# Kernel tuning notes

Hardware: AMD Instinct MI355X
Metric: run time of the kernel (lower is better)

Reference implementation:

```python
import jax, jax.numpy as jnp
import numpy as np

WINDOW = 16
VD = 6
HID = 16


def setup_inputs() -> dict:
    key = jax.random.key(0)
    ks = jax.random.split(key, 10)
    B, S = 256, 4096
    sc = 0.1
    return {
        "x": jax.random.normal(ks[0], (B, S, 2), jnp.float32),
        "h_0": jnp.zeros((B, HID), jnp.float32),
        "fir_I_w": jax.random.normal(ks[1], (VD, WINDOW), jnp.float32) * sc,
        "fir_Q_w": jax.random.normal(ks[2], (VD, WINDOW), jnp.float32) * sc,
        "W_fi_w": jax.random.normal(ks[3], (HID, 2 * VD), jnp.float32) * sc,
        "W_fi_b": jnp.zeros((HID,), jnp.float32),
        "W_fh_w": jax.random.normal(ks[4], (HID, HID), jnp.float32) * sc,
        "W_gi_w": jax.random.normal(ks[5], (HID, 2 * VD), jnp.float32) * sc,
        "W_gi_b": jnp.zeros((HID,), jnp.float32),
        "W_gh_w": jax.random.normal(ks[6], (HID, HID), jnp.float32) * sc,
        "W_out_I_w": jax.random.normal(ks[7], (1, HID), jnp.float32) * sc,
        "W_out_I_b": jnp.zeros((1,), jnp.float32),
        "W_out_Q_w": jax.random.normal(ks[8], (1, HID), jnp.float32) * sc,
        "W_out_Q_b": jnp.zeros((1,), jnp.float32),
    }


def _tile_theta(t, hidden):
    # pr_block replication logic for vd_units < hidden <= 3*vd_units cases
    if VD >= hidden:
        return t[..., :hidden]
    elif hidden <= 2 * VD:
        return jnp.concatenate([t, t[..., : hidden - VD]], axis=-1)
    else:
        return jnp.concatenate([t, t, t[..., : hidden - 2 * VD]], axis=-1)


def reference(x, h_0, fir_I_w, fir_Q_w, W_fi_w, W_fi_b, W_fh_w,
              W_gi_w, W_gi_b, W_gh_w, W_out_I_w, W_out_I_b,
              W_out_Q_w, W_out_Q_b):
    B, S, _ = x.shape
    # Causal sliding windows: window at t covers x[t-15 .. t] with zero pad.
    xp = jnp.concatenate([jnp.zeros((B, WINDOW - 1, 2), x.dtype), x], axis=1)
    idx = jnp.arange(S)[:, None] + jnp.arange(WINDOW)[None, :]  # (S, W)
    win = xp[:, idx, :]  # (B, S, W, 2)
    wI, wQ = win[..., 0], win[..., 1]  # (B, S, W)
    # Complex FIR filter
    I_fir = jnp.einsum('bsw,vw->bsv', wI, fir_I_w) - jnp.einsum('bsw,vw->bsv', wQ, fir_Q_w)
    Q_fir = jnp.einsum('bsw,vw->bsv', wI, fir_Q_w) + jnp.einsum('bsw,vw->bsv', wQ, fir_I_w)
    mag = jnp.sqrt(I_fir * I_fir + Q_fir * Q_fir) + 1e-8
    mag2 = mag * mag
    sin_t = Q_fir / mag
    cos_t = I_fir / mag
    # L = stack([mag, mag2], dim=2).view(B, S, 2*VD)
    L = jnp.stack([mag, mag2], axis=2).reshape(B, S, 2 * VD)
    # Precompute input contributions to gates; scan the recurrence.
    fi = jnp.einsum('bsl,hl->bsh', L, W_fi_w) + W_fi_b  # (B,S,H)
    gi = jnp.einsum('bsl,hl->bsh', L, W_gi_w) + W_gi_b

    def step(h, inp):
        fi_t, gi_t = inp
        f = jax.nn.sigmoid(fi_t + h @ W_fh_w.T)
        g = jnp.tanh(gi_t + h @ W_gh_w.T)
        h = f * h + (1.0 - f) * g
        return h, h

    _, h_seq = jax.lax.scan(step, h_0, (fi.transpose(1, 0, 2), gi.transpose(1, 0, 2)))
    h_seq = h_seq.transpose(1, 0, 2)  # (B, S, H)
    hidden = h_seq.shape[-1]
    cos_r = _tile_theta(cos_t, hidden)
    sin_r = _tile_theta(sin_t, hidden)
    I_rot = h_seq * cos_r
    Q_rot = h_seq * sin_r
    oI = I_rot @ W_out_I_w.T + W_out_I_b  # (B,S,1)
    oQ = Q_rot @ W_out_Q_w.T + W_out_Q_b
    out_I = oI - oQ
    out_Q = oQ + oI
    return jnp.concatenate([out_I, out_Q], axis=-1)
```

## Files before the change

kernel.cpp:

```cpp
#include <hip/hip_runtime.h>
#include <stdint.h>

#define DEV __device__ __forceinline__

constexpr int Bb   = 256;
constexpr int Ss   = 4096;
constexpr int HIDN = 16;
constexpr int VDN  = 6;
constexpr int WINN = 16;

constexpr int BPG   = 32;
constexpr int NG    = Bb / BPG;
constexpr int CHUNK = 16;
constexpr int WARM  = 16;
constexpr int NCH   = Ss / CHUNK;
constexpr int NPH   = (CHUNK + WARM) / 4;
constexpr int EPH   = WARM / 4;

constexpr size_t WSL_BYTES = (size_t)NG * Ss * 64 * 16;
constexpr size_t WSC_BYTES = (size_t)NG * Ss * BPG * 24;

typedef __fp16 h2v  __attribute__((ext_vector_type(2)));
typedef __fp16 f16x8 __attribute__((ext_vector_type(8)));
typedef float  f32x16 __attribute__((ext_vector_type(16)));

DEV uint32_t pk16(float a, float b) {
    h2v t = __builtin_amdgcn_cvt_pkrtz(a, b);
    uint32_t u; __builtin_memcpy(&u, &t, 4); return u;
}
DEV void up16(uint32_t u, float& a, float& b) {
    h2v t; __builtin_memcpy(&t, &u, 4);
    a = (float)t[0]; b = (float)t[1];
}
DEV f32x16 MF(const uint32_t* a, const uint32_t* b, f32x16 c) {
    f16x8 av, bv;
    __builtin_memcpy(&av, a, 16);
    __builtin_memcpy(&bv, b, 16);
    return __builtin_amdgcn_mfma_f32_32x32x16_f16(av, bv, c, 0, 0, 0);
}

template<int C> DEV int   dpp_i(int v)  { return __builtin_amdgcn_update_dpp(0, v, C, 0xF, 0xF, false); }
template<int C> DEV float dpp_f(float v){ return __int_as_float(dpp_i<C>(__float_as_int(v))); }
#define DPP_ALL(X) X(1,0x121) X(2,0x122) X(3,0x123) X(4,0x124) X(5,0x125) X(6,0x126) X(7,0x127) \
  X(8,0x128) X(9,0x129) X(10,0x12A) X(11,0x12B) X(12,0x12C) X(13,0x12D) X(14,0x12E) X(15,0x12F)

__global__ __launch_bounds__(256, 4) void boja_front(
    const float* __restrict__ x,
    const float* __restrict__ fIw, const float* __restrict__ fQw,
    uint4* __restrict__ wsl, uint2* __restrict__ wsc)
{
    __shared__ __align__(16) uint32_t lds[8 * 64 * 4];
    const int tid = threadIdx.x;
    const int tq  = tid & 7;
    const int b_  = tid >> 3;
    const int G   = blockIdx.y;
    const int t0  = blockIdx.x * 8;
    const int t   = t0 + tq;
    const int b   = G * BPG + b_;
    const int id  = b * Ss + t;
    const float2* x2 = (const float2*)x;

    float wI[WINN], wQ[WINN];
    if (t >= WINN - 1) {
#pragma unroll
        for (int w = 0; w < WINN; ++w) { float2 v = x2[id - 15 + w]; wI[w] = v.x; wQ[w] = v.y; }
    } else {
#pragma unroll
        for (int w = 0; w < WINN; ++w) {
            int ts = t - 15 + w;
            float2 v = (ts >= 0) ? x2[id - 15 + w] : make_float2(0.f, 0.f);
            wI[w] = v.x; wQ[w] = v.y;
        }
    }
    float aI[VDN], aQ[VDN];
#pragma unroll
    for (int v = 0; v < VDN; ++v) { aI[v] = 0.f; aQ[v] = 0.f; }
#pragma unroll
    for (int w = 0; w < WINN; ++w) {
#pragma unroll
        for (int v = 0; v < VDN; ++v) {
            aI[v] = fmaf( wI[w], fIw[v*16+w], aI[v]);
            aI[v] = fmaf(-wQ[w], fQw[v*16+w], aI[v]);
            aQ[v] = fmaf( wI[w], fQw[v*16+w], aQ[v]);
            aQ[v] = fmaf( wQ[w], fIw[v*16+w], aQ[v]);
        }
    }
    float L[12];
    uint32_t sc[6];
#pragma unroll
    for (int v = 0; v < VDN; ++v) {
        float m2 = fmaf(aI[v], aI[v], aQ[v]*aQ[v]);
        float mg = __builtin_amdgcn_sqrtf(m2) + 1e-8f;
        float iv = __builtin_amdgcn_rcpf(mg);
        L[v] = mg; L[6+v] = mg*mg;
        sc[v] = pk16(aI[v]*iv, aQ[v]*iv);
    }
    {
        const size_t cb = ((size_t)(G * Ss + t) * BPG + b_) * 3;
        wsc[cb+0] = make_uint2(sc[0], sc[1]);
        wsc[cb+1] = make_uint2(sc[2], sc[3]);
        wsc[cb+2] = make_uint2(sc[4], sc[5]);
    }
    const int lo = (tq*64 + b_) * 4, hi = (tq*64 + b_ + 32) * 4;
    lds[lo+0] = pk16(L[0], L[1]);  lds[lo+1] = pk16(L[2],  L[3]);
    lds[lo+2] = pk16(L[8], L[9]);  lds[lo+3] = pk16(L[10], L[11]);
    lds[hi+0] = pk16(L[4], L[5]);  lds[hi+1] = pk16(L[6],  L[7]);
    lds[hi+2] = 0x00003C00u;
    lds[hi+3] = 0u;
    __syncthreads();
#pragma unroll
    for (int r = 0; r < 2; ++r) {
        int idx = r*256 + tid;
        int tq2 = idx >> 6, lane = idx & 63;
        uint4 v = *(const uint4*)&lds[(tq2*64 + lane)*4];
        wsl[(size_t)(G*Ss + t0 + tq2) * 64 + lane] = v;
    }
}

__global__ __launch_bounds__(64, 2) void boja_rnn(
    const uint4* __restrict__ wsl, const uint2* __restrict__ wsc,
    const float* __restrict__ h0,
    const float* __restrict__ Wfh, const float* __restrict__ Wgh,
    const float* __restrict__ Wfi, const float* __restrict__ bfi,
    const float* __restrict__ Wgi, const float* __restrict__ bgi,
    const float* __restrict__ WoI, const float* __restrict__ boI,
    const float* __restrict__ WoQ, const float* __restrict__ boQ,
    float* __restrict__ out)
{
    const int l  = threadIdx.x;
    const int b_ = l & 31;
    const int h_ = l >> 5;
    const int G  = blockIdx.x & (NG - 1);
    const int ci = blockIdx.x >> 3;

    const int t_out0  = ci * CHUNK;
    const int t_start = t_out0 - WARM;
    const bool useh0  = (t_start <= 0);

    const float CF = -1.4426950408889634f;
    const float CG =  2.8853900817779268f;
    const int   m  = b_;
    const float sA = (m < 16) ? CF : CG;

    uint32_t a1[4], a2[4];
#pragma unroll
    for (int d = 0; d < 4; ++d) {
        float wv[2], uv[2];
#pragma unroll
        for (int q = 0; q < 2; ++q) {
            const int e = d*2 + q;
            const int k = (e & 3) + 8*(e >> 2) + 4*h_;
            wv[q] = ((m < 16) ? Wfh[m*16 + k] : Wgh[(m-16)*16 + k]) * sA;
            float u;
            if (k < 12)       u = ((m < 16) ? Wfi[m*12 + k] : Wgi[(m-16)*12 + k]) * sA;
            else if (k == 12) u = ((m < 16) ? bfi[m] : bgi[m-16]) * sA;
            else              u = 0.0f;
            uv[q] = u;
        }
        a1[d] = pk16(wv[0], wv[1]);
        a2[d] = pk16(uv[0], uv[1]);
    }

    float woi[8], woq[8];
#pragma unroll
    for (int r = 0; r < 8; ++r) {
        const int j = (r & 3) + 8*(r >> 2) + 4*h_;
        woi[r] = WoI[j]; woq[r] = WoQ[j];
    }
    const float bo_i = boI[0], bo_q = boQ[0];

    float h0r[8];
    if (useh0) {
        const float* hp = h0 + (size_t)(G*BPG + b_) * HIDN;
        float4 p = *(const float4*)(hp + 4*h_);
        float4 q = *(const float4*)(hp + 8 + 4*h_);
        h0r[0]=p.x; h0r[1]=p.y; h0r[2]=p.z; h0r[3]=p.w;
        h0r[4]=q.x; h0r[5]=q.y; h0r[6]=q.z; h0r[7]=q.w;
    }
    float hreg[8];
#pragma unroll
    for (int r = 0; r < 8; ++r) hreg[r] = 0.0f;
    uint32_t b1[4];
    b1[0]=0u; b1[1]=0u; b1[2]=0u; b1[3]=0u;

    f32x16 zero16;
#pragma unroll
    for (int i = 0; i < 16; ++i) zero16[i] = 0.0f;

    const uint4* lp = wsl + (size_t)G * Ss * 64 + l;
    const uint2* cp = wsc + ((size_t)G * Ss * BPG + b_) * 3;
    float2* outp = (float2*)out + (size_t)(G*BPG + b_) * Ss;

    uint4 LB[3][4];
    uint2 CB[2][4][3];

    auto loadL = [&](uint4 (&B)[4], int tb) {
#pragma unroll
        for (int s = 0; s < 4; ++s) {
            int tq2 = tb + s; tq2 = (tq2 < 0) ? 0 : tq2;
            B[s] = lp[(size_t)tq2 * 64];
        }
    };
    auto loadC = [&](uint2 (&C)[4][3], int tb) {
#pragma unroll
        for (int s = 0; s < 4; ++s)
#pragma unroll
            for (int k = 0; k < 3; ++k)
                C[s][k] = cp[(size_t)(tb + s) * (BPG*3) + k];
    };

    loadL(LB[0], t_start);
    loadL(LB[1], t_start + 4);

#define PHASE(P) { \
    const int tb = t_start + 4*(P); \
    if ((P) + 2 < NPH) loadL(LB[((P)+2)%3], t_start + 4*((P)+2)); \
    if ((P) + 1 >= EPH && (P) + 1 < NPH) loadC(CB[((P)+1)&1], t_start + 4*((P)+1)); \
    f32x16 accL = MF(a2, (const uint32_t*)&LB[(P)%3][0], zero16); \
    float ob[8]; \
    _Pragma("unroll") \
    for (int s = 0; s < 4; ++s) { \
        if (useh0 && tb + s == 0) { \
            _Pragma("unroll") for (int r = 0; r < 8; ++r) hreg[r] = h0r[r]; \
            b1[0]=pk16(hreg[0],hreg[1]); b1[1]=pk16(hreg[2],hreg[3]); \
            b1[2]=pk16(hreg[4],hreg[5]); b1[3]=pk16(hreg[6],hreg[7]); \
        } \
        f32x16 acc = MF(a1, b1, accL); \
        if (s < 3) accL = MF(a2, (const uint32_t*)&LB[(P)%3][s+1], zero16); \
        _Pragma("unroll") \
        for (int r = 0; r < 8; ++r) { \
            float f = __builtin_amdgcn_rcpf(1.0f + __builtin_amdgcn_exp2f(acc[r])); \
            float g = fmaf(-2.0f, __builtin_amdgcn_rcpf(1.0f + __builtin_amdgcn_exp2f(acc[r+8])), 1.0f); \
            hreg[r] = fmaf(f, hreg[r] - g, g); \
        } \
        b1[0]=pk16(hreg[0],hreg[1]); b1[1]=pk16(hreg[2],hreg[3]); \
        b1[2]=pk16(hreg[4],hreg[5]); b1[3]=pk16(hreg[6],hreg[7]); \
        if ((P) >= EPH) { \
            float cs6[6], sn6[6]; \
            up16(CB[(P)&1][s][0].x, cs6[0], sn6[0]); up16(CB[(P)&1][s][0].y, cs6[1], sn6[1]); \
            up16(CB[(P)&1][s][1].x, cs6[2], sn6[2]); up16(CB[(P)&1][s][1].y, cs6[3], sn6[3]); \
            up16(CB[(P)&1][s][2].x, cs6[4], sn6[4]); up16(CB[(P)&1][s][2].y, cs6[5], sn6[5]); \
            float oI = bo_i, oQ = bo_q; \
            const bool hb = (h_ != 0); \
            { \
                float c0,sn0; \
                c0 = hb?cs6[4]:cs6[0]; sn0 = hb?sn6[4]:sn6[0]; oI = fmaf(hreg[0]*c0, woi[0], oI); oQ = fmaf(hreg[0]*sn0, woq[0], oQ); \
                c0 = hb?cs6[5]:cs6[1]; sn0 = hb?sn6[5]:sn6[1]; oI = fmaf(hreg[1]*c0, woi[1], oI); oQ = fmaf(hreg[1]*sn0, woq[1], oQ); \
                c0 = hb?cs6[0]:cs6[2]; sn0 = hb?sn6[0]:sn6[2]; oI = fmaf(hreg[2]*c0, woi[2], oI); oQ = fmaf(hreg[2]*sn0, woq[2], oQ); \
                c0 = hb?cs6[1]:cs6[3]; sn0 = hb?sn6[1]:sn6[3]; oI = fmaf(hreg[3]*c0, woi[3], oI); oQ = fmaf(hreg[3]*sn0, woq[3], oQ); \
                c0 = hb?cs6[0]:cs6[2]; sn0 = hb?sn6[0]:sn6[2]; oI = fmaf(hreg[4]*c0, woi[4], oI); oQ = fmaf(hreg[4]*sn0, woq[4], oQ); \
                c0 = hb?cs6[1]:cs6[3]; sn0 = hb?sn6[1]:sn6[3]; oI = fmaf(hreg[5]*c0, woi[5], oI); oQ = fmaf(hreg[5]*sn0, woq[5], oQ); \
                c0 = hb?cs6[2]:cs6[4]; sn0 = hb?sn6[2]:sn6[4]; oI = fmaf(hreg[6]*c0, woi[6], oI); oQ = fmaf(hreg[6]*sn0, woq[6], oQ); \
                c0 = hb?cs6[3]:cs6[5]; sn0 = hb?sn6[3]:sn6[5]; oI = fmaf(hreg[7]*c0, woi[7], oI); oQ = fmaf(hreg[7]*sn0, woq[7], oQ); \
            } \
            oI += __shfl_xor(oI, 32, 64); \
            oQ += __shfl_xor(oQ, 32, 64); \
            ob[s*2] = oI - oQ; ob[s*2+1] = oI + oQ; \
        } \
    } \
    if ((P) >= EPH && l < 32) { \
        float4* po = (float4*)(outp + tb); \
        po[0] = make_float4(ob[0], ob[1], ob[2], ob[3]); \
        po[1] = make_float4(ob[4], ob[5], ob[6], ob[7]); \
    } \
}

    PHASE(0)  PHASE(1)  PHASE(2)  PHASE(3)
    PHASE(4)  PHASE(5)  PHASE(6)  PHASE(7)
#undef PHASE
}

__global__ __launch_bounds__(64, 2) void bojanet_v2(
    const float* __restrict__ x,   const float* __restrict__ h0,
    const float* __restrict__ fIw, const float* __restrict__ fQw,
    const float* __restrict__ Wfi, const float* __restrict__ bfi,
    const float* __restrict__ Wfh, const float* __restrict__ Wgi,
    const float* __restrict__ bgi, const float* __restrict__ Wgh,
    const float* __restrict__ WoI, const float* __restrict__ boI,
    const float* __restrict__ WoQ, const float* __restrict__ boQ,
    float* __restrict__ out)
{
    constexpr int FCH = 128, FWR = 64, FSB = 16;
    __shared__ __align__(16) float s_fi[FSB * 80];
    __shared__ __align__(16) float s_gi[FSB * 80];
    __shared__ __align__(16) float s_h [FSB * 68];
    __shared__ float s_sc[4 * 12 * 17];

    const int lane = threadIdx.x;
    const int j  = lane & 15;
    const int bl = lane >> 4;
    const int ci = blockIdx.x;
    const int b0 = blockIdx.y * 4;
    const int t_out0  = ci * FCH;
    const int t_start = ci ? (t_out0 - FWR) : 0;
    const int t_end   = t_out0 + FCH;

    int c[16]; c[0] = j;
#define CSET(K,CTL) c[K] = dpp_i<CTL>(j);
    DPP_ALL(CSET)
#undef CSET
    float wf[16], wg[16];
#pragma unroll
    for (int k = 0; k < 16; ++k) { wf[k] = Wfh[j*16 + c[k]]; wg[k] = Wgh[j*16 + c[k]]; }

    float h = (ci == 0) ? h0[(b0 + bl) * HIDN + j] : 0.0f;
    const float2* x2   = (const float2*)x + (size_t)(b0 + bl) * Ss;
    float2*       out2 = (float2*)out     + (size_t)(b0 + bl) * Ss;

    for (int tb = t_start; tb < t_end; tb += FSB) {
        const bool emit = (tb >= t_out0);
        {
            const int tg = tb + j;
            float wI[WINN], wQ[WINN];
            if (tb >= WINN - 1) {
#pragma unroll
                for (int w = 0; w < WINN; ++w) { float2 v = x2[tg - 15 + w]; wI[w] = v.x; wQ[w] = v.y; }
            } else {
#pragma unroll
                for (int w = 0; w < WINN; ++w) {
                    int ts = tg - 15 + w;
                    float2 v = (ts >= 0) ? x2[ts] : make_float2(0.f, 0.f);
                    wI[w] = v.x; wQ[w] = v.y;
                }
            }
            float aI[VDN], aQ[VDN];
#pragma unroll
            for (int v = 0; v < VDN; ++v) { aI[v] = 0.f; aQ[v] = 0.f; }
#pragma unroll
            for (int w = 0; w < WINN; ++w) {
#pragma unroll
                for (int v = 0; v < VDN; ++v) {
                    aI[v] = fmaf( wI[w], fIw[v*16+w], aI[v]);
                    aI[v] = fmaf(-wQ[w], fQw[v*16+w], aI[v]);
                    aQ[v] = fmaf( wI[w], fQw[v*16+w], aQ[v]);
                    aQ[v] = fmaf( wQ[w], fIw[v*16+w], aQ[v]);
                }
            }
            float L[12];
#pragma unroll
            for (int v = 0; v < VDN; ++v) {
                float m2 = fmaf(aI[v], aI[v], aQ[v]*aQ[v]);
                float mg = __builtin_amdgcn_sqrtf(m2) + 1e-8f;
                L[v] = mg; L[6+v] = mg*mg;
                if (emit) {
                    float iv = __builtin_amdgcn_rcpf(mg);
                    s_sc[(bl*12 + v  )*17 + j] = aI[v] * iv;
                    s_sc[(bl*12 + 6+v)*17 + j] = aQ[v] * iv;
                }
            }
            float fi[16], gi[16];
#pragma unroll
            for (int k = 0; k < 16; ++k) { fi[k] = bfi[k]; gi[k] = bgi[k]; }
#pragma unroll
            for (int ll = 0; ll < 12; ++ll) {
#pragma unroll
                for (int k = 0; k < 16; ++k) {
                    fi[k] = fmaf(L[ll], Wfi[k*12+ll], fi[k]);
                    gi[k] = fmaf(L[ll], Wgi[k*12+ll], gi[k]);
                }
            }
            float* pf = &s_fi[j*80 + bl*20];
            float* pg = &s_gi[j*80 + bl*20];
#pragma unroll
            for (int q = 0; q < 4; ++q) {
                *(float4*)(pf + 4*q) = make_float4(fi[4*q], fi[4*q+1], fi[4*q+2], fi[4*q+3]);
                *(float4*)(pg + 4*q) = make_float4(gi[4*q], gi[4*q+1], gi[4*q+2], gi[4*q+3]);
            }
        }
        __asm__ volatile("s_waitcnt lgkmcnt(0)" ::: "memory");
        {
            const int rb = bl*20 + j;
            float pf0 = s_fi[rb], pf1 = s_fi[80 + rb];
            float pg0 = s_gi[rb], pg1 = s_gi[80 + rb];
#pragma unroll
            for (int tt = 0; tt < FSB; ++tt) {
                const int nx = (tt + 2 < FSB) ? tt + 2 : FSB - 1;
                float pfn = s_fi[nx*80 + rb];
                float pgn = s_gi[nx*80 + rb];
                float hr[16]; hr[0] = h;
#define HSET(K,CTL) hr[K] = dpp_f<CTL>(h);
                DPP_ALL(HSET)
#undef HSET
                float af0 = pf0, af1 = 0.f, ag0 = pg0, ag1 = 0.f;
#pragma unroll
                for (int k = 0; k < 8; ++k) {
                    af0 = fmaf(wf[k],   hr[k],   af0);
                    ag0 = fmaf(wg[k],   hr[k],   ag0);
                    af1 = fmaf(wf[k+8], hr[k+8], af1);
                    ag1 = fmaf(wg[k+8], hr[k+8], ag1);
                }
                float zf = af0 + af1, zg = ag0 + ag1;
                float f = __builtin_amdgcn_rcpf(1.0f + __builtin_amdgcn_exp2f(zf * -1.4426950408889634f));
                float g = fmaf(-2.0f, __builtin_amdgcn_rcpf(1.0f + __builtin_amdgcn_exp2f(zg * 2.8853900817779268f)), 1.0f);
                h = fmaf(f, h - g, g);
                s_h[tt*68 + bl*16 + j] = h;
                pf0 = pf1; pf1 = pfn; pg0 = pg1; pg1 = pgn;
            }
        }
        __asm__ volatile("s_waitcnt lgkmcnt(0)" ::: "memory");
        if (emit) {
            const int tg = tb + j;
            float hv[16];
#pragma unroll
            for (int q = 0; q < 4; ++q) {
                float4 t4 = *(const float4*)&s_h[j*68 + bl*16 + 4*q];
                hv[4*q] = t4.x; hv[4*q+1] = t4.y; hv[4*q+2] = t4.z; hv[4*q+3] = t4.w;
            }
            float cs[12];
#pragma unroll
            for (int k = 0; k < 12; ++k) cs[k] = s_sc[(bl*12 + k)*17 + j];
            float oI = boI[0], oQ = boQ[0];
#pragma unroll
            for (int k = 0; k < 16; ++k) {
                int v = (k < 6) ? k : ((k < 12) ? k - 6 : k - 12);
                oI = fmaf(hv[k]*cs[v],   WoI[k], oI);
                oQ = fmaf(hv[k]*cs[6+v], WoQ[k], oQ);
            }
            out2[tg] = make_float2(oI - oQ, oI + oQ);
        }
        __asm__ volatile("s_waitcnt lgkmcnt(0)" ::: "memory");
    }
}

extern "C" void kernel_launch(void* const* d_in, const int* in_sizes, int n_in,
                              void* d_out, int out_size, void* d_ws, size_t ws_size,
                              hipStream_t stream) {
    const float* x   = (const float*)d_in[0];
    const float* h0  = (const float*)d_in[1];
    const float* fIw = (const float*)d_in[2];
    const float* fQw = (const float*)d_in[3];
    const float* Wfi = (const float*)d_in[4];
    const float* bfi = (const float*)d_in[5];
    const float* Wfh = (const float*)d_in[6];
    const float* Wgi = (const float*)d_in[7];
    const float* bgi = (const float*)d_in[8];
    const float* Wgh = (const float*)d_in[9];
    const float* WoI = (const float*)d_in[10];
    const float* boI = (const float*)d_in[11];
    const float* WoQ = (const float*)d_in[12];
    const float* boQ = (const float*)d_in[13];
    float* out = (float*)d_out;

    if (ws_size >= WSL_BYTES + WSC_BYTES) {
        uint4* wsl = (uint4*)d_ws;
        uint2* wsc = (uint2*)((char*)d_ws + WSL_BYTES);
        boja_front<<<dim3(Ss/8, NG), 256, 0, stream>>>(x, fIw, fQw, wsl, wsc);
        boja_rnn<<<dim3(NG * NCH), 64, 0, stream>>>(
            wsl, wsc, h0, Wfh, Wgh, Wfi, bfi, Wgi, bgi, WoI, boI, WoQ, boQ, out);
    } else {
        bojanet_v2<<<dim3(32, Bb / 4), 64, 0, stream>>>(
            x, h0, fIw, fQw, Wfi, bfi, Wfh, Wgi, bgi, Wgh, WoI, boI, WoQ, boQ, out);
    }
}
```

Measured before the change: 48.83 us.

## Switch RNN recurrence to 16x16x32 MFMA with 16-batch groups and compact workspace

Replaces the 32x32x16 MFMA recurrence (32 batches per wave, f and g gates stacked) with 16x16x32 MFMAs over 16 batches per wave, issuing separate f and g MFMAs. The front kernel now writes a tighter fp16 workspace (48 uint2 per timestep instead of 64 uint4) and stages the cos/sin data through LDS so global writes are coalesced. Doubling the group count doubles the number of RNN blocks, giving more parallel waves for the latency-bound sequential chain. The cost is four MFMAs per step instead of two, plus an extra shuffle stage in the output reduction.

```diff
diff --git a/kernel.cpp b/kernel.cpp
--- a/kernel.cpp
+++ b/kernel.cpp
@@ -9,7 +9,7 @@
 constexpr int VDN  = 6;
 constexpr int WINN = 16;
 
-constexpr int BPG   = 32;
+constexpr int BPG   = 16;
 constexpr int NG    = Bb / BPG;
 constexpr int CHUNK = 16;
 constexpr int WARM  = 16;
@@ -17,12 +17,12 @@
 constexpr int NPH   = (CHUNK + WARM) / 4;
 constexpr int EPH   = WARM / 4;
 
-constexpr size_t WSL_BYTES = (size_t)NG * Ss * 64 * 16;
+constexpr size_t WSL_BYTES = (size_t)NG * Ss * 48 * 8;
 constexpr size_t WSC_BYTES = (size_t)NG * Ss * BPG * 24;
 
-typedef __fp16 h2v  __attribute__((ext_vector_type(2)));
+typedef __fp16 h2v   __attribute__((ext_vector_type(2)));
 typedef __fp16 f16x8 __attribute__((ext_vector_type(8)));
-typedef float  f32x16 __attribute__((ext_vector_type(16)));
+typedef float  f32x4 __attribute__((ext_vector_type(4)));
 
 DEV uint32_t pk16(float a, float b) {
     h2v t = __builtin_amdgcn_cvt_pkrtz(a, b);
@@ -32,11 +32,11 @@
     h2v t; __builtin_memcpy(&t, &u, 4);
     a = (float)t[0]; b = (float)t[1];
 }
-DEV f32x16 MF(const uint32_t* a, const uint32_t* b, f32x16 c) {
+DEV f32x4 MF16(const uint32_t* a, const uint32_t* b, f32x4 c) {
     f16x8 av, bv;
     __builtin_memcpy(&av, a, 16);
     __builtin_memcpy(&bv, b, 16);
-    return __builtin_amdgcn_mfma_f32_32x32x16_f16(av, bv, c, 0, 0, 0);
+    return __builtin_amdgcn_mfma_f32_16x16x32_f16(av, bv, c, 0, 0, 0);
 }
 
 template<int C> DEV int   dpp_i(int v)  { return __builtin_amdgcn_update_dpp(0, v, C, 0xF, 0xF, false); }
@@ -44,18 +44,20 @@
 #define DPP_ALL(X) X(1,0x121) X(2,0x122) X(3,0x123) X(4,0x124) X(5,0x125) X(6,0x126) X(7,0x127) \
   X(8,0x128) X(9,0x129) X(10,0x12A) X(11,0x12B) X(12,0x12C) X(13,0x12D) X(14,0x12E) X(15,0x12F)
 
-__global__ __launch_bounds__(256, 4) void boja_front(
+__global__ __launch_bounds__(256, 4) void boja_front16(
     const float* __restrict__ x,
     const float* __restrict__ fIw, const float* __restrict__ fQw,
-    uint4* __restrict__ wsl, uint2* __restrict__ wsc)
+    uint2* __restrict__ wsl, uint2* __restrict__ wsc)
 {
-    __shared__ __align__(16) uint32_t lds[8 * 64 * 4];
+    __shared__ __align__(8) uint2 lsl[16 * 48];
+    __shared__ __align__(8) uint2 lsc[16 * 48];
+
     const int tid = threadIdx.x;
-    const int tq  = tid & 7;
-    const int b_  = tid >> 3;
+    const int tl  = tid & 15;
+    const int b_  = tid >> 4;
     const int G   = blockIdx.y;
-    const int t0  = blockIdx.x * 8;
-    const int t   = t0 + tq;
+    const int t0  = blockIdx.x * 16;
+    const int t   = t0 + tl;
     const int b   = G * BPG + b_;
     const int id  = b * Ss + t;
     const float2* x2 = (const float2*)x;
@@ -85,40 +87,34 @@
             aQ[v] = fmaf( wQ[w], fIw[v*16+w], aQ[v]);
         }
     }
-    float L[12];
-    uint32_t sc[6];
+    float mg[VDN], mq[VDN];
+    uint32_t sc[VDN];
 #pragma unroll
     for (int v = 0; v < VDN; ++v) {
         float m2 = fmaf(aI[v], aI[v], aQ[v]*aQ[v]);
-        float mg = __builtin_amdgcn_sqrtf(m2) + 1e-8f;
-        float iv = __builtin_amdgcn_rcpf(mg);
-        L[v] = mg; L[6+v] = mg*mg;
+        mg[v] = __builtin_amdgcn_sqrtf(m2) + 1e-8f;
+        mq[v] = mg[v] * mg[v];
+        float iv = __builtin_amdgcn_rcpf(mg[v]);
         sc[v] = pk16(aI[v]*iv, aQ[v]*iv);
     }
-    {
-        const size_t cb = ((size_t)(G * Ss + t) * BPG + b_) * 3;
-        wsc[cb+0] = make_uint2(sc[0], sc[1]);
-        wsc[cb+1] = make_uint2(sc[2], sc[3]);
-        wsc[cb+2] = make_uint2(sc[4], sc[5]);
-    }
-    const int lo = (tq*64 + b_) * 4, hi = (tq*64 + b_ + 32) * 4;
-    lds[lo+0] = pk16(L[0], L[1]);  lds[lo+1] = pk16(L[2],  L[3]);
-    lds[lo+2] = pk16(L[8], L[9]);  lds[lo+3] = pk16(L[10], L[11]);
-    lds[hi+0] = pk16(L[4], L[5]);  lds[hi+1] = pk16(L[6],  L[7]);
-    lds[hi+2] = 0x00003C00u;
-    lds[hi+3] = 0u;
+    lsl[tl*48 +  0 + b_] = make_uint2(pk16(mg[0], mg[1]), pk16(mg[2], mg[3]));
+    lsl[tl*48 + 16 + b_] = make_uint2(pk16(mg[4], mg[5]), pk16(mq[0], mq[1]));
+    lsl[tl*48 + 32 + b_] = make_uint2(pk16(mq[2], mq[3]), pk16(mq[4], mq[5]));
+    lsc[tl*48 + b_*3 + 0] = make_uint2(sc[0], sc[1]);
+    lsc[tl*48 + b_*3 + 1] = make_uint2(sc[2], sc[3]);
+    lsc[tl*48 + b_*3 + 2] = make_uint2(sc[4], sc[5]);
     __syncthreads();
 #pragma unroll
-    for (int r = 0; r < 2; ++r) {
+    for (int r = 0; r < 3; ++r) {
         int idx = r*256 + tid;
-        int tq2 = idx >> 6, lane = idx & 63;
-        uint4 v = *(const uint4*)&lds[(tq2*64 + lane)*4];
-        wsl[(size_t)(G*Ss + t0 + tq2) * 64 + lane] = v;
-    }
-}
-
-__global__ __launch_bounds__(64, 2) void boja_rnn(
-    const uint4* __restrict__ wsl, const uint2* __restrict__ wsc,
+        int tq2 = idx / 48, e = idx - tq2*48;
+        wsl[(size_t)(G*Ss + t0 + tq2) * 48 + e] = lsl[idx];
+        wsc[(size_t)(G*Ss + t0 + tq2) * 48 + e] = lsc[idx];
+    }
+}
+
+__global__ __launch_bounds__(64, 4) void boja_rnn16(
+    const uint2* __restrict__ wsl, const uint2* __restrict__ wsc,
     const float* __restrict__ h0,
     const float* __restrict__ Wfh, const float* __restrict__ Wgh,
     const float* __restrict__ Wfi, const float* __restrict__ bfi,
@@ -128,10 +124,10 @@
     float* __restrict__ out)
 {
     const int l  = threadIdx.x;
-    const int b_ = l & 31;
-    const int h_ = l >> 5;
+    const int b_ = l & 15;
+    const int q  = l >> 4;
     const int G  = blockIdx.x & (NG - 1);
-    const int ci = blockIdx.x >> 3;
+    const int ci = blockIdx.x >> 4;
 
     const int t_out0  = ci * CHUNK;
     const int t_start = t_out0 - WARM;
@@ -139,74 +135,60 @@
 
     const float CF = -1.4426950408889634f;
     const float CG =  2.8853900817779268f;
-    const int   m  = b_;
-    const float sA = (m < 16) ? CF : CG;
-
-    uint32_t a1[4], a2[4];
-#pragma unroll
-    for (int d = 0; d < 4; ++d) {
-        float wv[2], uv[2];
-#pragma unroll
-        for (int q = 0; q < 2; ++q) {
-            const int e = d*2 + q;
-            const int k = (e & 3) + 8*(e >> 2) + 4*h_;
-            wv[q] = ((m < 16) ? Wfh[m*16 + k] : Wgh[(m-16)*16 + k]) * sA;
-            float u;
-            if (k < 12)       u = ((m < 16) ? Wfi[m*12 + k] : Wgi[(m-16)*12 + k]) * sA;
-            else if (k == 12) u = ((m < 16) ? bfi[m] : bgi[m-16]) * sA;
-            else              u = 0.0f;
-            uv[q] = u;
-        }
-        a1[d] = pk16(wv[0], wv[1]);
-        a2[d] = pk16(uv[0], uv[1]);
-    }
-
-    float woi[8], woq[8];
-#pragma unroll
-    for (int r = 0; r < 8; ++r) {
-        const int j = (r & 3) + 8*(r >> 2) + 4*h_;
-        woi[r] = WoI[j]; woq[r] = WoQ[j];
-    }
+
+    uint32_t a1f[4] = {0,0,0,0}, a1g[4] = {0,0,0,0};
+    uint32_t a2f[4] = {0,0,0,0}, a2g[4] = {0,0,0,0};
+    const int m_ = b_;
+#pragma unroll
+    for (int d = 0; d < 2; ++d) {
+        const int k0 = 4*q + 2*d, k1 = k0 + 1;
+        a1f[d] = pk16(Wfh[m_*16 + k0]*CF, Wfh[m_*16 + k1]*CF);
+        a1g[d] = pk16(Wgh[m_*16 + k0]*CG, Wgh[m_*16 + k1]*CG);
+        auto uf = [&](int k)->float { return (k < 12) ? Wfi[m_*12 + k] : ((k == 12) ? bfi[m_] : 0.f); };
+        auto ug = [&](int k)->float { return (k < 12) ? Wgi[m_*12 + k] : ((k == 12) ? bgi[m_] : 0.f); };
+        a2f[d] = pk16(uf(k0)*CF, uf(k1)*CF);
+        a2g[d] = pk16(ug(k0)*CG, ug(k1)*CG);
+    }
+
+    float woi[4], woq[4];
+#pragma unroll
+    for (int r = 0; r < 4; ++r) { woi[r] = WoI[4*q + r]; woq[r] = WoQ[4*q + r]; }
     const float bo_i = boI[0], bo_q = boQ[0];
 
-    float h0r[8];
+    float h0r[4];
     if (useh0) {
-        const float* hp = h0 + (size_t)(G*BPG + b_) * HIDN;
-        float4 p = *(const float4*)(hp + 4*h_);
-        float4 q = *(const float4*)(hp + 8 + 4*h_);
+        float4 p = *(const float4*)(h0 + (size_t)(G*BPG + b_) * HIDN + 4*q);
         h0r[0]=p.x; h0r[1]=p.y; h0r[2]=p.z; h0r[3]=p.w;
-        h0r[4]=q.x; h0r[5]=q.y; h0r[6]=q.z; h0r[7]=q.w;
-    }
-    float hreg[8];
-#pragma unroll
-    for (int r = 0; r < 8; ++r) hreg[r] = 0.0f;
-    uint32_t b1[4];
-    b1[0]=0u; b1[1]=0u; b1[2]=0u; b1[3]=0u;
-
-    f32x16 zero16;
-#pragma unroll
-    for (int i = 0; i < 16; ++i) zero16[i] = 0.0f;
-
-    const uint4* lp = wsl + (size_t)G * Ss * 64 + l;
-    const uint2* cp = wsc + ((size_t)G * Ss * BPG + b_) * 3;
+    }
+    float hreg[4] = {0.f, 0.f, 0.f, 0.f};
+    uint32_t b1[4] = {0u, 0u, 0u, 0u};
+    f32x4 zero4; zero4[0]=0.f; zero4[1]=0.f; zero4[2]=0.f; zero4[3]=0.f;
+
+    const uint2* lp = wsl + (size_t)G * Ss * 48 + (q < 3 ? q : 0) * 16 + b_;
+    const uint2* cpb = wsc + (size_t)G * Ss * 48 + b_ * 3;
+    const int o0 = (q == 1) ? 2 : ((q == 2) ? 1 : 0);
+    const int o1 = (q == 2) ? 2 : ((q == 1) ? 0 : 1);
     float2* outp = (float2*)out + (size_t)(G*BPG + b_) * Ss;
 
-    uint4 LB[3][4];
-    uint2 CB[2][4][3];
-
-    auto loadL = [&](uint4 (&B)[4], int tb) {
+    uint2 LB[3][4];
+    uint2 CB[2][4][2];
+
+    auto loadL = [&](uint2 (&B)[4], int tb) {
 #pragma unroll
         for (int s = 0; s < 4; ++s) {
             int tq2 = tb + s; tq2 = (tq2 < 0) ? 0 : tq2;
-            B[s] = lp[(size_t)tq2 * 64];
+            uint2 v = lp[(size_t)tq2 * 48];
+            if (q == 3) v = make_uint2(0x00003C00u, 0u);
+            B[s] = v;
         }
     };
-    auto loadC = [&](uint2 (&C)[4][3], int tb) {
-#pragma unroll
-        for (int s = 0; s < 4; ++s)
-#pragma unroll
-            for (int k = 0; k < 3; ++k)
-                C[s][k] = cp[(size_t)(tb + s) * (BPG*3) + k];
+    auto loadC = [&](uint2 (&C)[4][2], int tb) {
+#pragma unroll
+        for (int s = 0; s < 4; ++s) {
+            const uint2* base = cpb + (size_t)(tb + s) * 48;
+            C[s][0] = base[o0];
+            C[s][1] = base[o1];
+        }
     };
 
     loadL(LB[0], t_start);
@@ -216,49 +198,38 @@
     const int tb = t_start + 4*(P); \
     if ((P) + 2 < NPH) loadL(LB[((P)+2)%3], t_start + 4*((P)+2)); \
     if ((P) + 1 >= EPH && (P) + 1 < NPH) loadC(CB[((P)+1)&1], t_start + 4*((P)+1)); \
-    f32x16 accL = MF(a2, (const uint32_t*)&LB[(P)%3][0], zero16); \
     float ob[8]; \
     _Pragma("unroll") \
     for (int s = 0; s < 4; ++s) { \
         if (useh0 && tb + s == 0) { \
-            _Pragma("unroll") for (int r = 0; r < 8; ++r) hreg[r] = h0r[r]; \
-            b1[0]=pk16(hreg[0],hreg[1]); b1[1]=pk16(hreg[2],hreg[3]); \
-            b1[2]=pk16(hreg[4],hreg[5]); b1[3]=pk16(hreg[6],hreg[7]); \
+            _Pragma("unroll") for (int r = 0; r < 4; ++r) hreg[r] = h0r[r]; \
+            b1[0] = pk16(hreg[0], hreg[1]); b1[1] = pk16(hreg[2], hreg[3]); \
         } \
-        f32x16 acc = MF(a1, b1, accL); \
-        if (s < 3) accL = MF(a2, (const uint32_t*)&LB[(P)%3][s+1], zero16); \
+        uint32_t Lfr[4]; Lfr[0] = LB[(P)%3][s].x; Lfr[1] = LB[(P)%3][s].y; Lfr[2] = 0u; Lfr[3] = 0u; \
+        f32x4 accf = MF16(a2f, Lfr, zero4); \
+        f32x4 accg = MF16(a2g, Lfr, zero4); \
+        accf = MF16(a1f, b1, accf); \
+        accg = MF16(a1g, b1, accg); \
         _Pragma("unroll") \
-        for (int r = 0; r < 8; ++r) { \
-            float f = __builtin_amdgcn_rcpf(1.0f + __builtin_amdgcn_exp2f(acc[r])); \
-            float g = fmaf(-2.0f, __builtin_amdgcn_rcpf(1.0f + __builtin_amdgcn_exp2f(acc[r+8])), 1.0f); \
+        for (int r = 0; r < 4; ++r) { \
+            float f = __builtin_amdgcn_rcpf(1.0f + __builtin_amdgcn_exp2f(accf[r])); \
+            float g = fmaf(-2.0f, __builtin_amdgcn_rcpf(1.0f + __builtin_amdgcn_exp2f(accg[r])), 1.0f); \
             hreg[r] = fmaf(f, hreg[r] - g, g); \
         } \
-        b1[0]=pk16(hreg[0],hreg[1]); b1[1]=pk16(hreg[2],hreg[3]); \
-        b1[2]=pk16(hreg[4],hreg[5]); b1[3]=pk16(hreg[6],hreg[7]); \
+        b1[0] = pk16(hreg[0], hreg[1]); b1[1] = pk16(hreg[2], hreg[3]); \
         if ((P) >= EPH) { \
-            float cs6[6], sn6[6]; \
-            up16(CB[(P)&1][s][0].x, cs6[0], sn6[0]); up16(CB[(P)&1][s][0].y, cs6[1], sn6[1]); \
-            up16(CB[(P)&1][s][1].x, cs6[2], sn6[2]); up16(CB[(P)&1][s][1].y, cs6[3], sn6[3]); \
-            up16(CB[(P)&1][s][2].x, cs6[4], sn6[4]); up16(CB[(P)&1][s][2].y, cs6[5], sn6[5]); \
-            float oI = bo_i, oQ = bo_q; \
-            const bool hb = (h_ != 0); \
-            { \
-                float c0,sn0; \
-                c0 = hb?cs6[4]:cs6[0]; sn0 = hb?sn6[4]:sn6[0]; oI = fmaf(hreg[0]*c0, woi[0], oI); oQ = fmaf(hreg[0]*sn0, woq[0], oQ); \
-                c0 = hb?cs6[5]:cs6[1]; sn0 = hb?sn6[5]:sn6[1]; oI = fmaf(hreg[1]*c0, woi[1], oI); oQ = fmaf(hreg[1]*sn0, woq[1], oQ); \
-                c0 = hb?cs6[0]:cs6[2]; sn0 = hb?sn6[0]:sn6[2]; oI = fmaf(hreg[2]*c0, woi[2], oI); oQ = fmaf(hreg[2]*sn0, woq[2], oQ); \
-                c0 = hb?cs6[1]:cs6[3]; sn0 = hb?sn6[1]:sn6[3]; oI = fmaf(hreg[3]*c0, woi[3], oI); oQ = fmaf(hreg[3]*sn0, woq[3], oQ); \
-                c0 = hb?cs6[0]:cs6[2]; sn0 = hb?sn6[0]:sn6[2]; oI = fmaf(hreg[4]*c0, woi[4], oI); oQ = fmaf(hreg[4]*sn0, woq[4], oQ); \
-                c0 = hb?cs6[1]:cs6[3]; sn0 = hb?sn6[1]:sn6[3]; oI = fmaf(hreg[5]*c0, woi[5], oI); oQ = fmaf(hreg[5]*sn0, woq[5], oQ); \
-                c0 = hb?cs6[2]:cs6[4]; sn0 = hb?sn6[2]:sn6[4]; oI = fmaf(hreg[6]*c0, woi[6], oI); oQ = fmaf(hreg[6]*sn0, woq[6], oQ); \
-                c0 = hb?cs6[3]:cs6[5]; sn0 = hb?sn6[3]:sn6[5]; oI = fmaf(hreg[7]*c0, woi[7], oI); oQ = fmaf(hreg[7]*sn0, woq[7], oQ); \
-            } \
-            oI += __shfl_xor(oI, 32, 64); \
-            oQ += __shfl_xor(oQ, 32, 64); \
+            float c0,s0,c1,s1,c2,s2,c3,s3; \
+            up16(CB[(P)&1][s][0].x, c0, s0); up16(CB[(P)&1][s][0].y, c1, s1); \
+            up16(CB[(P)&1][s][1].x, c2, s2); up16(CB[(P)&1][s][1].y, c3, s3); \
+            float oI = hreg[0]*c0*woi[0] + hreg[1]*c1*woi[1] + hreg[2]*c2*woi[2] + hreg[3]*c3*woi[3]; \
+            float oQ = hreg[0]*s0*woq[0] + hreg[1]*s1*woq[1] + hreg[2]*s2*woq[2] + hreg[3]*s3*woq[3]; \
+            oI += __shfl_xor(oI, 16, 64); oI += __shfl_xor(oI, 32, 64); \
+            oQ += __shfl_xor(oQ, 16, 64); oQ += __shfl_xor(oQ, 32, 64); \
+            oI += bo_i; oQ += bo_q; \
             ob[s*2] = oI - oQ; ob[s*2+1] = oI + oQ; \
         } \
     } \
-    if ((P) >= EPH && l < 32) { \
+    if ((P) >= EPH && l < 16) { \
         float4* po = (float4*)(outp + tb); \
         po[0] = make_float4(ob[0], ob[1], ob[2], ob[3]); \
         po[1] = make_float4(ob[4], ob[5], ob[6], ob[7]); \
@@ -362,9 +333,9 @@
             float* pf = &s_fi[j*80 + bl*20];
             float* pg = &s_gi[j*80 + bl*20];
 #pragma unroll
-            for (int q = 0; q < 4; ++q) {
-                *(float4*)(pf + 4*q) = make_float4(fi[4*q], fi[4*q+1], fi[4*q+2], fi[4*q+3]);
-                *(float4*)(pg + 4*q) = make_float4(gi[4*q], gi[4*q+1], gi[4*q+2], gi[4*q+3]);
+            for (int qq = 0; qq < 4; ++qq) {
+                *(float4*)(pf + 4*qq) = make_float4(fi[4*qq], fi[4*qq+1], fi[4*qq+2], fi[4*qq+3]);
+                *(float4*)(pg + 4*qq) = make_float4(gi[4*qq], gi[4*qq+1], gi[4*qq+2], gi[4*qq+3]);
             }
         }
         __asm__ volatile("s_waitcnt lgkmcnt(0)" ::: "memory");
@@ -402,9 +373,9 @@
             const int tg = tb + j;
             float hv[16];
 #pragma unroll
-            for (int q = 0; q < 4; ++q) {
-                float4 t4 = *(const float4*)&s_h[j*68 + bl*16 + 4*q];
-                hv[4*q] = t4.x; hv[4*q+1] = t4.y; hv[4*q+2] = t4.z; hv[4*q+3] = t4.w;
+            for (int qq = 0; qq < 4; ++qq) {
+                float4 t4 = *(const float4*)&s_h[j*68 + bl*16 + 4*qq];
+                hv[4*qq] = t4.x; hv[4*qq+1] = t4.y; hv[4*qq+2] = t4.z; hv[4*qq+3] = t4.w;
             }
             float cs[12];
 #pragma unroll
@@ -442,10 +413,10 @@
     float* out = (float*)d_out;
 
     if (ws_size >= WSL_BYTES + WSC_BYTES) {
-        uint4* wsl = (uint4*)d_ws;
+        uint2* wsl = (uint2*)d_ws;
         uint2* wsc = (uint2*)((char*)d_ws + WSL_BYTES);
-        boja_front<<<dim3(Ss/8, NG), 256, 0, stream>>>(x, fIw, fQw, wsl, wsc);
-        boja_rnn<<<dim3(NG * NCH), 64, 0, stream>>>(
+        boja_front16<<<dim3(Ss/16, NG), 256, 0, stream>>>(x, fIw, fQw, wsl, wsc);
+        boja_rnn16<<<dim3(NG * NCH), 64, 0, stream>>>(
             wsl, wsc, h0, Wfh, Wgh, Wfi, bfi, Wgi, bgi, WoI, boI, WoQ, boQ, out);
     } else {
         bojanet_v2<<<dim3(32, Bb / 4), 64, 0, stream>>>(
```

Result: slower. 50.42 us (+3.3%).

## Halve L workspace by storing magnitudes only and shrink RNN chunks

Applied to the files above, without the earlier changes.

The front kernel now writes 16 bytes per (t,batch) of packed fp16 magnitudes plus one mag² pair, rather than a 64-lane padded layout holding both mag and mag². The RNN kernel rebuilds the MFMA B-operand in registers, squaring the fp16 magnitudes with packed half multiplies and inserting the bias one/zero. The chunk length drops from 16 to 8 with the same warm-up, so there are twice as many blocks, and occupancy is raised to 4. Prefetch depth grows to three phases ahead. The aim is to cut workspace traffic and add parallelism, at the cost of proportionally more redundant warm-up recurrence work and fp16 rounding on mag² computed from an already-rounded magnitude.

```diff
diff --git a/kernel.cpp b/kernel.cpp
--- a/kernel.cpp
+++ b/kernel.cpp
@@ -11,16 +11,16 @@
 
 constexpr int BPG   = 32;
 constexpr int NG    = Bb / BPG;
-constexpr int CHUNK = 16;
+constexpr int CHUNK = 8;
 constexpr int WARM  = 16;
 constexpr int NCH   = Ss / CHUNK;
 constexpr int NPH   = (CHUNK + WARM) / 4;
 constexpr int EPH   = WARM / 4;
 
-constexpr size_t WSL_BYTES = (size_t)NG * Ss * 64 * 16;
+constexpr size_t WSL_BYTES = (size_t)NG * Ss * BPG * 16;
 constexpr size_t WSC_BYTES = (size_t)NG * Ss * BPG * 24;
 
-typedef __fp16 h2v  __attribute__((ext_vector_type(2)));
+typedef __fp16 h2v   __attribute__((ext_vector_type(2)));
 typedef __fp16 f16x8 __attribute__((ext_vector_type(8)));
 typedef float  f32x16 __attribute__((ext_vector_type(16)));
 
@@ -31,6 +31,11 @@
 DEV void up16(uint32_t u, float& a, float& b) {
     h2v t; __builtin_memcpy(&t, &u, 4);
     a = (float)t[0]; b = (float)t[1];
+}
+DEV uint32_t sqpk(uint32_t u) {
+    h2v t; __builtin_memcpy(&t, &u, 4);
+    t = t * t;
+    uint32_t r; __builtin_memcpy(&r, &t, 4); return r;
 }
 DEV f32x16 MF(const uint32_t* a, const uint32_t* b, f32x16 c) {
     f16x8 av, bv;
@@ -49,7 +54,7 @@
     const float* __restrict__ fIw, const float* __restrict__ fQw,
     uint4* __restrict__ wsl, uint2* __restrict__ wsc)
 {
-    __shared__ __align__(16) uint32_t lds[8 * 64 * 4];
+    __shared__ __align__(16) uint4 lsl[256];
     const int tid = threadIdx.x;
     const int tq  = tid & 7;
     const int b_  = tid >> 3;
@@ -85,14 +90,13 @@
             aQ[v] = fmaf( wQ[w], fIw[v*16+w], aQ[v]);
         }
     }
-    float L[12];
-    uint32_t sc[6];
+    float mg[VDN];
+    uint32_t sc[VDN];
 #pragma unroll
     for (int v = 0; v < VDN; ++v) {
         float m2 = fmaf(aI[v], aI[v], aQ[v]*aQ[v]);
-        float mg = __builtin_amdgcn_sqrtf(m2) + 1e-8f;
-        float iv = __builtin_amdgcn_rcpf(mg);
-        L[v] = mg; L[6+v] = mg*mg;
+        mg[v] = __builtin_amdgcn_sqrtf(m2) + 1e-8f;
+        float iv = __builtin_amdgcn_rcpf(mg[v]);
         sc[v] = pk16(aI[v]*iv, aQ[v]*iv);
     }
     {
@@ -101,23 +105,16 @@
         wsc[cb+1] = make_uint2(sc[2], sc[3]);
         wsc[cb+2] = make_uint2(sc[4], sc[5]);
     }
-    const int lo = (tq*64 + b_) * 4, hi = (tq*64 + b_ + 32) * 4;
-    lds[lo+0] = pk16(L[0], L[1]);  lds[lo+1] = pk16(L[2],  L[3]);
-    lds[lo+2] = pk16(L[8], L[9]);  lds[lo+3] = pk16(L[10], L[11]);
-    lds[hi+0] = pk16(L[4], L[5]);  lds[hi+1] = pk16(L[6],  L[7]);
-    lds[hi+2] = 0x00003C00u;
-    lds[hi+3] = 0u;
+    lsl[tq*32 + b_] = make_uint4(pk16(mg[0], mg[1]), pk16(mg[2], mg[3]),
+                                 pk16(mg[4], mg[5]), pk16(mg[0]*mg[0], mg[1]*mg[1]));
     __syncthreads();
-#pragma unroll
-    for (int r = 0; r < 2; ++r) {
-        int idx = r*256 + tid;
-        int tq2 = idx >> 6, lane = idx & 63;
-        uint4 v = *(const uint4*)&lds[(tq2*64 + lane)*4];
-        wsl[(size_t)(G*Ss + t0 + tq2) * 64 + lane] = v;
-    }
-}
-
-__global__ __launch_bounds__(64, 2) void boja_rnn(
+    {
+        const int tq2 = tid >> 5, b2 = tid & 31;
+        wsl[((size_t)(G*Ss + t0 + tq2)) * BPG + b2] = lsl[tid];
+    }
+}
+
+__global__ __launch_bounds__(64, 4) void boja_rnn(
     const uint4* __restrict__ wsl, const uint2* __restrict__ wsc,
     const float* __restrict__ h0,
     const float* __restrict__ Wfh, const float* __restrict__ Wgh,
@@ -187,18 +184,18 @@
 #pragma unroll
     for (int i = 0; i < 16; ++i) zero16[i] = 0.0f;
 
-    const uint4* lp = wsl + (size_t)G * Ss * 64 + l;
+    const uint4* lp = wsl + (size_t)G * Ss * BPG + b_;
     const uint2* cp = wsc + ((size_t)G * Ss * BPG + b_) * 3;
     float2* outp = (float2*)out + (size_t)(G*BPG + b_) * Ss;
 
-    uint4 LB[3][4];
+    uint4 LB[4][4];
     uint2 CB[2][4][3];
 
     auto loadL = [&](uint4 (&B)[4], int tb) {
 #pragma unroll
         for (int s = 0; s < 4; ++s) {
             int tq2 = tb + s; tq2 = (tq2 < 0) ? 0 : tq2;
-            B[s] = lp[(size_t)tq2 * 64];
+            B[s] = lp[(size_t)tq2 * BPG];
         }
     };
     auto loadC = [&](uint2 (&C)[4][3], int tb) {
@@ -211,13 +208,23 @@
 
     loadL(LB[0], t_start);
     loadL(LB[1], t_start + 4);
+    loadL(LB[2], t_start + 8);
 
 #define PHASE(P) { \
     const int tb = t_start + 4*(P); \
-    if ((P) + 2 < NPH) loadL(LB[((P)+2)%3], t_start + 4*((P)+2)); \
+    if ((P) + 3 < NPH) loadL(LB[((P)+3)&3], t_start + 4*((P)+3)); \
     if ((P) + 1 >= EPH && (P) + 1 < NPH) loadC(CB[((P)+1)&1], t_start + 4*((P)+1)); \
-    f32x16 accL = MF(a2, (const uint32_t*)&LB[(P)%3][0], zero16); \
     float ob[8]; \
+    uint32_t fw[4][4]; \
+    _Pragma("unroll") \
+    for (int s = 0; s < 4; ++s) { \
+        uint4 v = LB[(P)&3][s]; \
+        fw[s][0] = h_ ? v.z : v.x; \
+        fw[s][1] = h_ ? v.w : v.y; \
+        fw[s][2] = h_ ? 0x00003C00u : sqpk(v.y); \
+        fw[s][3] = h_ ? 0u : sqpk(v.z); \
+    } \
+    f32x16 accL = MF(a2, fw[0], zero16); \
     _Pragma("unroll") \
     for (int s = 0; s < 4; ++s) { \
         if (useh0 && tb + s == 0) { \
@@ -226,7 +233,7 @@
             b1[2]=pk16(hreg[4],hreg[5]); b1[3]=pk16(hreg[6],hreg[7]); \
         } \
         f32x16 acc = MF(a1, b1, accL); \
-        if (s < 3) accL = MF(a2, (const uint32_t*)&LB[(P)%3][s+1], zero16); \
+        if (s < 3) accL = MF(a2, fw[s+1], zero16); \
         _Pragma("unroll") \
         for (int r = 0; r < 8; ++r) { \
             float f = __builtin_amdgcn_rcpf(1.0f + __builtin_amdgcn_exp2f(acc[r])); \
@@ -265,8 +272,8 @@
     } \
 }
 
-    PHASE(0)  PHASE(1)  PHASE(2)  PHASE(3)
-    PHASE(4)  PHASE(5)  PHASE(6)  PHASE(7)
+    PHASE(0)  PHASE(1)  PHASE(2)
+    PHASE(3)  PHASE(4)  PHASE(5)
 #undef PHASE
 }
 
@@ -362,9 +369,9 @@
             float* pf = &s_fi[j*80 + bl*20];
             float* pg = &s_gi[j*80 + bl*20];
 #pragma unroll
-            for (int q = 0; q < 4; ++q) {
-                *(float4*)(pf + 4*q) = make_float4(fi[4*q], fi[4*q+1], fi[4*q+2], fi[4*q+3]);
-                *(float4*)(pg + 4*q) = make_float4(gi[4*q], gi[4*q+1], gi[4*q+2], gi[4*q+3]);
+            for (int qq = 0; qq < 4; ++qq) {
+                *(float4*)(pf + 4*qq) = make_float4(fi[4*qq], fi[4*qq+1], fi[4*qq+2], fi[4*qq+3]);
+                *(float4*)(pg + 4*qq) = make_float4(gi[4*qq], gi[4*qq+1], gi[4*qq+2], gi[4*qq+3]);
             }
         }
         __asm__ volatile("s_waitcnt lgkmcnt(0)" ::: "memory");
@@ -402,9 +409,9 @@
             const int tg = tb + j;
             float hv[16];
 #pragma unroll
-            for (int q = 0; q < 4; ++q) {
-                float4 t4 = *(const float4*)&s_h[j*68 + bl*16 + 4*q];
-                hv[4*q] = t4.x; hv[4*q+1] = t4.y; hv[4*q+2] = t4.z; hv[4*q+3] = t4.w;
+            for (int qq = 0; qq < 4; ++qq) {
+                float4 t4 = *(const float4*)&s_h[j*68 + bl*16 + 4*qq];
+                hv[4*qq] = t4.x; hv[4*qq+1] = t4.y; hv[4*qq+2] = t4.z; hv[4*qq+3] = t4.w;
             }
             float cs[12];
 #pragma unroll
```

Measured after the change: 60.61 us. +24.1%, slower.
